# Kernel optimization log

Hardware: AMD Instinct MI355X
Metric: run time of the kernel (lower is better)

The kernel has to match this reference:

```python
import jax, jax.numpy as jnp
import numpy as np

N_HEADS = 16
NEG_INF = float('-inf')


def setup_inputs() -> dict:
    key = jax.random.key(0)
    ks = jax.random.split(key, 8)
    B, S, D = 8, 1024, 1024
    inp = {
        'q': jax.random.normal(ks[0], (B, S, D), jnp.float32),
        'k': jax.random.normal(ks[1], (B, S, D), jnp.float32),
        'v': jax.random.normal(ks[2], (B, S, D), jnp.float32),
        'key_padding_mask': jnp.zeros((B, S), bool),
        'Wq': jax.random.normal(ks[3], (D, D), jnp.float32) / np.sqrt(D),
        'bq': jnp.zeros((D,), jnp.float32),
        'Wk': jax.random.normal(ks[4], (D, D), jnp.float32) / np.sqrt(D),
        'bk': jnp.zeros((D,), jnp.float32),
        'Wv': jax.random.normal(ks[5], (D, D), jnp.float32) / np.sqrt(D),
        'bv': jnp.zeros((D,), jnp.float32),
        'Wo': jax.random.normal(ks[6], (D, D), jnp.float32) / np.sqrt(D),
        'bo': jnp.zeros((D,), jnp.float32),
    }
    return inp


def reference(q, k, v, key_padding_mask, Wq, bq, Wk, bk, Wv, bv, Wo, bo):
    B, T, D = q.shape
    S = k.shape[1]
    H = N_HEADS
    dh = D // H
    causal = True

    # projections (torch Linear: x @ W.T + b)
    qh = (q @ Wq.T + bq).reshape(B, T, H, dh).transpose(0, 2, 1, 3)  # b h t d
    kh = (k @ Wk.T + bk).reshape(B, S, H, dh).transpose(0, 2, 1, 3)  # b h s d
    vh = (v @ Wv.T + bv).reshape(B, S, H, dh).transpose(0, 2, 1, 3)  # b h s d

    s = jnp.einsum('bhtd,bhsd->bhts', qh, kh) / jnp.sqrt(jnp.asarray(dh, s_dtype(qh)))
    s = jnp.where(key_padding_mask[:, None, None, :], NEG_INF, s)
    if causal:
        cmask = jnp.triu(jnp.full((T, S), NEG_INF, s.dtype), 1)
        s = s + cmask[None, None]
    a = jax.nn.softmax(s.astype(jnp.float32), axis=-1).astype(s.dtype)
    o = jnp.einsum('bhts,bhsd->bhtd', a, vh)
    o = o.transpose(0, 2, 1, 3).reshape(B, T, D)
    return o @ Wo.T + bo


def s_dtype(x):
    return x.dtype
```

## Files before the change

kernel.cpp:

```cpp
#include <hip/hip_runtime.h>
#include <hip/hip_bf16.h>

typedef unsigned short u16;
typedef unsigned int u32;
typedef __attribute__((ext_vector_type(8))) short bf16x8;
typedef __attribute__((ext_vector_type(4))) float f32x4;

#define LOG2E 1.44269504088896340736f


__device__ inline u16 f2bf(float f) {
  union { float f; u32 u; } v; v.f = f;
  u32 r = v.u + 0x7fffu + ((v.u >> 16) & 1u);
  return (u16)(r >> 16);
}

__device__ inline void gload_lds16(const u16* g, u16* l) {
  __builtin_amdgcn_global_load_lds(
      (const __attribute__((address_space(1))) u32*)g,
      (__attribute__((address_space(3))) u32*)l, 16, 0, 0);
}


__global__ void cvt_multi(const float4* __restrict__ s0, const float4* __restrict__ s1,
                          const float4* __restrict__ s2, const float4* __restrict__ s3,
                          ushort4* __restrict__ d0, ushort4* __restrict__ d1,
                          ushort4* __restrict__ d2, ushort4* __restrict__ d3, int n4) {
  const float4* s; ushort4* d;
  switch (blockIdx.y) {
    case 0: s = s0; d = d0; break;
    case 1: s = s1; d = d1; break;
    case 2: s = s2; d = d2; break;
    default: s = s3; d = d3; break;
  }
  int stride = gridDim.x * blockDim.x;
  for (int i = blockIdx.x * blockDim.x + threadIdx.x; i < n4; i += stride) {
    float4 v = s[i];
    ushort4 o;
    o.x = f2bf(v.x); o.y = f2bf(v.y); o.z = f2bf(v.z); o.w = f2bf(v.w);
    d[i] = o;
  }
}


__global__ void mask_flags(const unsigned char* __restrict__ mask,
                           unsigned char* __restrict__ flags) {
  int t = threadIdx.x;
  if (t >= 128) return;
  const uint4* p = (const uint4*)(mask + (size_t)t * 64);
  uint4 a = p[0], b = p[1], c = p[2], d = p[3];
  u32 v = a.x | a.y | a.z | a.w | b.x | b.y | b.z | b.w |
          c.x | c.y | c.z | c.w | d.x | d.y | d.z | d.w;
  flags[t] = v ? 1 : 0;
}


template<int MODE>
__global__ __launch_bounds__(256) void gemm_nt_bf16(
    const u16* __restrict__ A, const u16* __restrict__ Bt,
    const float* __restrict__ bias, void* __restrict__ Cout,
    int M, int N, int K) {
  constexpr int BK = 32;
  __shared__ u16 sA[2][128 * BK];
  __shared__ u16 sB[2][128 * BK];

  const int tid = threadIdx.x;
  const int lane = tid & 63;
  const int wave = tid >> 6;
  const int g = lane >> 4;
  const int r = lane & 15;
  const int wr = wave >> 1, wc = wave & 1;
  const int m0 = blockIdx.y * 128, n0 = blockIdx.x * 128;

  f32x4 acc[4][4] = {};

  auto stage = [&](int buf, int kt) {
    const int k0 = kt * BK;
#pragma unroll
    for (int i = 0; i < 2; ++i) {
      int c = tid + i * 256;
      int row = c >> 2, cc = c & 3;
      gload_lds16(A + (size_t)(m0 + row) * K + k0 + cc * 8, &sA[buf][0] + c * 8);
    }
#pragma unroll
    for (int i = 0; i < 2; ++i) {
      int c = tid + i * 256;
      int row = c >> 2, cc = c & 3;
      gload_lds16(Bt + (size_t)(n0 + row) * K + k0 + cc * 8, &sB[buf][0] + c * 8);
    }
  };

  stage(0, 0);
  const int NT = K / BK;
  for (int kt = 0; kt < NT; ++kt) {
    __syncthreads();
    if (kt + 1 < NT) stage((kt + 1) & 1, kt + 1);
    const u16* a_base = &sA[kt & 1][0];
    const u16* b_base = &sB[kt & 1][0];
    bf16x8 avf[4], bvf[4];
#pragma unroll
    for (int i = 0; i < 4; ++i) {
      avf[i] = *(const bf16x8*)(a_base + (wr * 64 + i * 16 + r) * BK + g * 8);
      bvf[i] = *(const bf16x8*)(b_base + (wc * 64 + i * 16 + r) * BK + g * 8);
    }
#pragma unroll
    for (int i = 0; i < 4; ++i)
#pragma unroll
      for (int j = 0; j < 4; ++j)
        acc[i][j] = __builtin_amdgcn_mfma_f32_16x16x32_bf16(avf[i], bvf[j], acc[i][j], 0, 0, 0);
  }

#pragma unroll
  for (int i = 0; i < 4; ++i) {
    int rowb = m0 + wr * 64 + i * 16 + g * 4;
#pragma unroll
    for (int j = 0; j < 4; ++j) {
      int col = n0 + wc * 64 + j * 16 + r;
      float bv = bias[col];
#pragma unroll
      for (int q = 0; q < 4; ++q) {
        int row = rowb + q;
        float v = acc[i][j][q] + bv;
        if (MODE == 0) {
          ((float*)Cout)[(size_t)row * N + col] = v;
        } else if (MODE == 1) {
          int b = row >> 10, t = row & 1023, h = col >> 6, d = col & 63;
          ((u16*)Cout)[((((size_t)b * 16 + h) << 10) + t) * 64 + d] = f2bf(v);
        } else {
          int b = row >> 10, s = row & 1023, h = col >> 6, d = col & 63;
          ((u16*)Cout)[(((size_t)b * 16 + h) * 64 + d) * 1024 + s] = f2bf(v);
        }
      }
    }
  }
}


__global__ __launch_bounds__(256) void gemm_qkv(
    const u16* __restrict__ Aq, const u16* __restrict__ Ak, const u16* __restrict__ Av,
    const u16* __restrict__ Wqb, const u16* __restrict__ Wkb, const u16* __restrict__ Wvb,
    const float* __restrict__ bqp, const float* __restrict__ bkp, const float* __restrict__ bvp,
    u16* __restrict__ Qh, u16* __restrict__ Kh, u16* __restrict__ Vt,
    int M, int N, int K) {
  constexpr int BK = 32;
  __shared__ u16 sA[2][128 * BK];
  __shared__ u16 sB[2][128 * BK];

  const int z = blockIdx.z;
  const u16* A  = (z == 0) ? Aq : (z == 1) ? Ak : Av;
  const u16* Bt = (z == 0) ? Wqb : (z == 1) ? Wkb : Wvb;
  const float* bias = (z == 0) ? bqp : (z == 1) ? bkp : bvp;

  const int tid = threadIdx.x;
  const int lane = tid & 63;
  const int wave = tid >> 6;
  const int g = lane >> 4;
  const int r = lane & 15;
  const int wr = wave >> 1, wc = wave & 1;
  const int m0 = blockIdx.y * 128, n0 = blockIdx.x * 128;

  f32x4 acc[4][4] = {};

  auto stage = [&](int buf, int kt) {
    const int k0 = kt * BK;
#pragma unroll
    for (int i = 0; i < 2; ++i) {
      int c = tid + i * 256;
      int row = c >> 2, cc = c & 3;
      gload_lds16(A + (size_t)(m0 + row) * K + k0 + cc * 8, &sA[buf][0] + c * 8);
    }
#pragma unroll
    for (int i = 0; i < 2; ++i) {
      int c = tid + i * 256;
      int row = c >> 2, cc = c & 3;
      gload_lds16(Bt + (size_t)(n0 + row) * K + k0 + cc * 8, &sB[buf][0] + c * 8);
    }
  };

  stage(0, 0);
  const int NT = K / BK;
  for (int kt = 0; kt < NT; ++kt) {
    __syncthreads();
    if (kt + 1 < NT) stage((kt + 1) & 1, kt + 1);
    const u16* a_base = &sA[kt & 1][0];
    const u16* b_base = &sB[kt & 1][0];
    bf16x8 avf[4], bvf[4];
#pragma unroll
    for (int i = 0; i < 4; ++i) {
      avf[i] = *(const bf16x8*)(a_base + (wr * 64 + i * 16 + r) * BK + g * 8);
      bvf[i] = *(const bf16x8*)(b_base + (wc * 64 + i * 16 + r) * BK + g * 8);
    }
#pragma unroll
    for (int i = 0; i < 4; ++i)
#pragma unroll
      for (int j = 0; j < 4; ++j)
        acc[i][j] = __builtin_amdgcn_mfma_f32_16x16x32_bf16(avf[i], bvf[j], acc[i][j], 0, 0, 0);
  }

#pragma unroll
  for (int i = 0; i < 4; ++i) {
    int rowb = m0 + wr * 64 + i * 16 + g * 4;
#pragma unroll
    for (int j = 0; j < 4; ++j) {
      int col = n0 + wc * 64 + j * 16 + r;
      float bv = bias[col];
#pragma unroll
      for (int q = 0; q < 4; ++q) {
        int row = rowb + q;
        float v = acc[i][j][q] + bv;
        int b = row >> 10, t = row & 1023, h = col >> 6, d = col & 63;
        if (z <= 1) {
          u16* dst = (z == 0) ? Qh : Kh;
          dst[((((size_t)b * 16 + h) << 10) + t) * 64 + d] = f2bf(v);
        } else {
          Vt[(((size_t)b * 16 + h) * 64 + d) * 1024 + t] = f2bf(v);
        }
      }
    }
  }
}


__global__ __launch_bounds__(256) void attn_fwd(
    const u16* __restrict__ Qh, const u16* __restrict__ Kh,
    const u16* __restrict__ Vt, const unsigned char* __restrict__ mask,
    const unsigned char* __restrict__ padflags,
    u16* __restrict__ O) {
  constexpr int S = 1024, DH = 64;
  __shared__ u16 sK[2][64 * 64];
  __shared__ u16 sV[2][64 * 64];
  __shared__ u16 sP[4][16 * 64];

  const int tid = threadIdx.x, lane = tid & 63, wave = tid >> 6;
  const int g = lane >> 4, r = lane & 15;
  const int bh = blockIdx.x;
  const int qt = blockIdx.y;
  const int b = bh >> 4, h = bh & 15;
  const int qw = qt * 128 + wave * 32;

  bf16x8 qf[2][2];
#pragma unroll
  for (int u = 0; u < 2; ++u) {
    const u16* Qb = Qh + ((size_t)bh * S + qw + u * 16 + r) * DH;
    qf[u][0] = *(const bf16x8*)(Qb + g * 8);
    qf[u][1] = *(const bf16x8*)(Qb + 32 + g * 8);
  }

  f32x4 acc[2][4] = {};
  float mrun[2][4], lrun[2][4];
#pragma unroll
  for (int u = 0; u < 2; ++u)
#pragma unroll
    for (int i = 0; i < 4; ++i) { mrun[u][i] = -INFINITY; lrun[u][i] = 0.f; }

  auto stage = [&](int buf, int kvt) {
    const int s0k = kvt * 64;
#pragma unroll
    for (int i = 0; i < 2; ++i) {
      int c = tid + i * 256;
      int row = c >> 3;
      int cc = (c & 7) ^ (row & 7);
      gload_lds16(Kh + ((size_t)bh * S + s0k + row) * DH + cc * 8, &sK[buf][0] + c * 8);
      gload_lds16(Vt + ((size_t)bh * DH + row) * S + s0k + cc * 8, &sV[buf][0] + c * 8);
    }
  };

  const int NT = 2 * (qt + 1);
  stage(0, 0);
  for (int kvt = 0; kvt < NT; ++kvt) {
    __syncthreads();
    if (kvt + 1 < NT) stage((kvt + 1) & 1, kvt + 1);
    const int cur = kvt & 1;
    const int s0 = kvt * 64;
    const bool pad = padflags[b * 16 + (s0 >> 6)] != 0;
    const u16* Kb = &sK[cur][0];
    const u16* Vb = &sV[cur][0];
    u16* Pw = &sP[wave][0];

#pragma unroll
    for (int u = 0; u < 2; ++u) {
      const int qg = qw + u * 16;
      if (s0 > qg + 15) continue;
      const bool diag = (s0 + 63 > qg);

      f32x4 sc[4] = {};
#pragma unroll
      for (int ss = 0; ss < 4; ++ss) {
#pragma unroll
        for (int kc = 0; kc < 2; ++kc) {
          int krow = ss * 16 + r;
          int byteoff = krow * 128 + kc * 64 + g * 16;
          bf16x8 kf = *(const bf16x8*)((const char*)Kb + (byteoff ^ ((krow & 7) << 4)));
          sc[ss] = __builtin_amdgcn_mfma_f32_16x16x32_bf16(qf[u][kc], kf, sc[ss], 0, 0, 0);
        }
      }

      float sv[4][4];
      float pmax[4] = {-INFINITY, -INFINITY, -INFINITY, -INFINITY};
#pragma unroll
      for (int ss = 0; ss < 4; ++ss) {
        float padd = 0.f;
        if (pad) {
          int s_g = s0 + ss * 16 + r;
          if (mask[(size_t)b * S + s_g]) padd = -INFINITY;
        }
#pragma unroll
        for (int reg = 0; reg < 4; ++reg) {
          float v = sc[ss][reg] * (0.125f * LOG2E) + padd;
          if (diag) {
            int s_g = s0 + ss * 16 + r;
            int q_g = qg + g * 4 + reg;
            if (s_g > q_g) v = -INFINITY;
          }
          sv[ss][reg] = v;
          pmax[reg] = fmaxf(pmax[reg], v);
        }
      }
#pragma unroll
      for (int reg = 0; reg < 4; ++reg) {
        float m = pmax[reg];
        m = fmaxf(m, __shfl_xor(m, 1));
        m = fmaxf(m, __shfl_xor(m, 2));
        m = fmaxf(m, __shfl_xor(m, 4));
        m = fmaxf(m, __shfl_xor(m, 8));
        float newm = fmaxf(mrun[u][reg], m);
        float alpha = (newm == -INFINITY) ? 1.f : exp2f(mrun[u][reg] - newm);
        mrun[u][reg] = newm;
        float rs = 0.f;
#pragma unroll
        for (int ss = 0; ss < 4; ++ss) {
          float p = (newm == -INFINITY) ? 0.f : exp2f(sv[ss][reg] - newm);
          sv[ss][reg] = p;
          rs += p;
        }
        rs += __shfl_xor(rs, 1);
        rs += __shfl_xor(rs, 2);
        rs += __shfl_xor(rs, 4);
        rs += __shfl_xor(rs, 8);
        lrun[u][reg] = lrun[u][reg] * alpha + rs;
#pragma unroll
        for (int df = 0; df < 4; ++df) acc[u][df][reg] *= alpha;
      }

#pragma unroll
      for (int ss = 0; ss < 4; ++ss) {
#pragma unroll
        for (int reg = 0; reg < 4; ++reg) {
          int qrow = g * 4 + reg;
          int byteoff = qrow * 128 + (ss * 16 + r) * 2;
          *(u16*)((char*)Pw + (byteoff ^ ((qrow & 7) << 4))) = f2bf(sv[ss][reg]);
        }
      }

#pragma unroll
      for (int sc2 = 0; sc2 < 2; ++sc2) {
        int pbyte = r * 128 + sc2 * 64 + g * 16;
        bf16x8 pf = *(const bf16x8*)((const char*)Pw + (pbyte ^ ((r & 7) << 4)));
#pragma unroll
        for (int df = 0; df < 4; ++df) {
          int vrow = df * 16 + r;
          int vbyte = vrow * 128 + sc2 * 64 + g * 16;
          bf16x8 vf = *(const bf16x8*)((const char*)Vb + (vbyte ^ ((vrow & 7) << 4)));
          acc[u][df] = __builtin_amdgcn_mfma_f32_16x16x32_bf16(pf, vf, acc[u][df], 0, 0, 0);
        }
      }
    }
  }

#pragma unroll
  for (int u = 0; u < 2; ++u) {
#pragma unroll
    for (int reg = 0; reg < 4; ++reg) {
      float l = lrun[u][reg];
      float inv = (l > 0.f) ? 1.f / l : 0.f;
      int t = qw + u * 16 + g * 4 + reg;
#pragma unroll
      for (int df = 0; df < 4; ++df) {
        float vo = acc[u][df][reg] * inv;
        O[((size_t)b * 1024 + t) * 1024 + h * 64 + df * 16 + r] = f2bf(vo);
      }
    }
  }
}


extern "C" void kernel_launch(void* const* d_in, const int* in_sizes, int n_in,
                              void* d_out, int out_size, void* d_ws, size_t ws_size,
                              hipStream_t stream) {
  const float* q  = (const float*)d_in[0];
  const float* k  = (const float*)d_in[1];
  const float* v  = (const float*)d_in[2];
  const unsigned char* mask = (const unsigned char*)d_in[3];
  const float* Wq = (const float*)d_in[4];
  const float* bq = (const float*)d_in[5];
  const float* Wk = (const float*)d_in[6];
  const float* bk = (const float*)d_in[7];
  const float* Wv = (const float*)d_in[8];
  const float* bv = (const float*)d_in[9];
  const float* Wo = (const float*)d_in[10];
  const float* bo = (const float*)d_in[11];

  const int M = 8192, N = 1024, K = 1024;
  const size_t MB = 1u << 20;
  char* ws = (char*)d_ws;

  if (ws_size >= 104 * MB + 4096) {
    u16* Aq  = (u16*)(ws);
    u16* Ak  = (u16*)(ws + 16 * MB);
    u16* Av  = (u16*)(ws + 32 * MB);
    u16* Qh  = (u16*)(ws + 48 * MB);
    u16* Kh  = (u16*)(ws + 64 * MB);
    u16* Vt  = (u16*)(ws + 80 * MB);
    u16* Wqb = (u16*)(ws + 96 * MB);
    u16* Wkb = Wqb + (1u << 20);
    u16* Wvb = Wkb + (1u << 20);
    u16* Wob = Wvb + (1u << 20);
    unsigned char* flags = (unsigned char*)(ws + 104 * MB);
    u16* AttO = Aq;

    cvt_multi<<<dim3(1024, 3), 256, 0, stream>>>(
        (const float4*)q, (const float4*)k, (const float4*)v, (const float4*)q,
        (ushort4*)Aq, (ushort4*)Ak, (ushort4*)Av, (ushort4*)Aq, (M * K) / 4);
    cvt_multi<<<dim3(256, 4), 256, 0, stream>>>(
        (const float4*)Wq, (const float4*)Wk, (const float4*)Wv, (const float4*)Wo,
        (ushort4*)Wqb, (ushort4*)Wkb, (ushort4*)Wvb, (ushort4*)Wob, (N * K) / 4);
    mask_flags<<<1, 128, 0, stream>>>(mask, flags);

    gemm_qkv<<<dim3(N / 128, M / 128, 3), 256, 0, stream>>>(
        Aq, Ak, Av, Wqb, Wkb, Wvb, bq, bk, bv, Qh, Kh, Vt, M, N, K);

    attn_fwd<<<dim3(128, 8), 256, 0, stream>>>(Qh, Kh, Vt, mask, flags, AttO);

    gemm_nt_bf16<0><<<dim3(N / 128, M / 128), 256, 0, stream>>>(
        AttO, Wob, bo, (float*)d_out, M, N, K);
  } else {
    u16* wsA = (u16*)ws;
    u16* Qh  = (u16*)(ws + 16 * MB);
    u16* Kh  = (u16*)(ws + 32 * MB);
    u16* Vt  = (u16*)(ws + 48 * MB);
    u16* Wqb = (u16*)(ws + 64 * MB);
    u16* Wkb = Wqb + (1u << 20);
    u16* Wvb = Wkb + (1u << 20);
    u16* Wob = Wvb + (1u << 20);
    unsigned char* flags = (unsigned char*)(ws + 72 * MB);

    cvt_multi<<<dim3(256, 4), 256, 0, stream>>>(
        (const float4*)Wq, (const float4*)Wk, (const float4*)Wv, (const float4*)Wo,
        (ushort4*)Wqb, (ushort4*)Wkb, (ushort4*)Wvb, (ushort4*)Wob, (N * K) / 4);
    mask_flags<<<1, 128, 0, stream>>>(mask, flags);

    cvt_multi<<<dim3(1024, 1), 256, 0, stream>>>(
        (const float4*)q, (const float4*)q, (const float4*)q, (const float4*)q,
        (ushort4*)wsA, (ushort4*)wsA, (ushort4*)wsA, (ushort4*)wsA, (M * K) / 4);
    gemm_nt_bf16<1><<<dim3(N / 128, M / 128), 256, 0, stream>>>(wsA, Wqb, bq, Qh, M, N, K);
    cvt_multi<<<dim3(1024, 1), 256, 0, stream>>>(
        (const float4*)k, (const float4*)k, (const float4*)k, (const float4*)k,
        (ushort4*)wsA, (ushort4*)wsA, (ushort4*)wsA, (ushort4*)wsA, (M * K) / 4);
    gemm_nt_bf16<1><<<dim3(N / 128, M / 128), 256, 0, stream>>>(wsA, Wkb, bk, Kh, M, N, K);
    cvt_multi<<<dim3(1024, 1), 256, 0, stream>>>(
        (const float4*)v, (const float4*)v, (const float4*)v, (const float4*)v,
        (ushort4*)wsA, (ushort4*)wsA, (ushort4*)wsA, (ushort4*)wsA, (M * K) / 4);
    gemm_nt_bf16<2><<<dim3(N / 128, M / 128), 256, 0, stream>>>(wsA, Wvb, bv, Vt, M, N, K);

    attn_fwd<<<dim3(128, 8), 256, 0, stream>>>(Qh, Kh, Vt, mask, flags, wsA);

    gemm_nt_bf16<0><<<dim3(N / 128, M / 128), 256, 0, stream>>>(
        wsA, Wob, bo, (float*)d_out, M, N, K);
  }
}
```

Before: 261.1 us.

## Fold softmax scale into Q projection, use DPP reductions, reverse causal tile order

The softmax scale (1/sqrt(dh)·log2e) is now applied once in the Q projection epilogue instead of on every score element in the attention loop. The cross-lane row max/sum reductions switch from ds_swizzle-based shuffles to DPP row_shr moves. Causal query tiles are launched in reverse so the heavy tiles start first and load balances better. P is converted to bf16 by truncation instead of round-to-nearest, which adds a small precision bias. Scaling Q before rounding it to bf16 also changes rounding slightly.

```diff
diff --git a/kernel.cpp b/kernel.cpp
--- a/kernel.cpp
+++ b/kernel.cpp
@@ -7,6 +7,7 @@
 typedef __attribute__((ext_vector_type(4))) float f32x4;
 
 #define LOG2E 1.44269504088896340736f
+#define QSCALE (0.125f * LOG2E)
 
 
 __device__ inline u16 f2bf(float f) {
@@ -19,6 +20,27 @@
   __builtin_amdgcn_global_load_lds(
       (const __attribute__((address_space(1))) u32*)g,
       (__attribute__((address_space(3))) u32*)l, 16, 0, 0);
+}
+
+template<int CTRL>
+__device__ inline float dppmov(float x) {
+  int i = __builtin_bit_cast(int, x);
+  int r = __builtin_amdgcn_update_dpp(i, i, CTRL, 0xf, 0xf, false);
+  return __builtin_bit_cast(float, r);
+}
+__device__ inline float rowmax16(float v) {
+  v = fmaxf(v, dppmov<0x128>(v));
+  v = fmaxf(v, dppmov<0x124>(v));
+  v = fmaxf(v, dppmov<0x122>(v));
+  v = fmaxf(v, dppmov<0x121>(v));
+  return v;
+}
+__device__ inline float rowsum16(float v) {
+  v += dppmov<0x128>(v);
+  v += dppmov<0x124>(v);
+  v += dppmov<0x122>(v);
+  v += dppmov<0x121>(v);
+  return v;
 }
 
 
@@ -123,7 +145,8 @@
         float v = acc[i][j][q] + bv;
         if (MODE == 0) {
           ((float*)Cout)[(size_t)row * N + col] = v;
-        } else if (MODE == 1) {
+        } else if (MODE == 1 || MODE == 3) {
+          if (MODE == 3) v *= QSCALE;
           int b = row >> 10, t = row & 1023, h = col >> 6, d = col & 63;
           ((u16*)Cout)[((((size_t)b * 16 + h) << 10) + t) * 64 + d] = f2bf(v);
         } else {
@@ -209,9 +232,10 @@
         int row = rowb + q;
         float v = acc[i][j][q] + bv;
         int b = row >> 10, t = row & 1023, h = col >> 6, d = col & 63;
-        if (z <= 1) {
-          u16* dst = (z == 0) ? Qh : Kh;
-          dst[((((size_t)b * 16 + h) << 10) + t) * 64 + d] = f2bf(v);
+        if (z == 0) {
+          Qh[((((size_t)b * 16 + h) << 10) + t) * 64 + d] = f2bf(v * QSCALE);
+        } else if (z == 1) {
+          Kh[((((size_t)b * 16 + h) << 10) + t) * 64 + d] = f2bf(v);
         } else {
           Vt[(((size_t)b * 16 + h) * 64 + d) * 1024 + t] = f2bf(v);
         }
@@ -234,7 +258,7 @@
   const int tid = threadIdx.x, lane = tid & 63, wave = tid >> 6;
   const int g = lane >> 4, r = lane & 15;
   const int bh = blockIdx.x;
-  const int qt = blockIdx.y;
+  const int qt = (int)gridDim.y - 1 - (int)blockIdx.y;
   const int b = bh >> 4, h = bh & 15;
   const int qw = qt * 128 + wave * 32;
 
@@ -306,7 +330,7 @@
         }
 #pragma unroll
         for (int reg = 0; reg < 4; ++reg) {
-          float v = sc[ss][reg] * (0.125f * LOG2E) + padd;
+          float v = sc[ss][reg] + padd;
           if (diag) {
             int s_g = s0 + ss * 16 + r;
             int q_g = qg + g * 4 + reg;
@@ -318,11 +342,7 @@
       }
 #pragma unroll
       for (int reg = 0; reg < 4; ++reg) {
-        float m = pmax[reg];
-        m = fmaxf(m, __shfl_xor(m, 1));
-        m = fmaxf(m, __shfl_xor(m, 2));
-        m = fmaxf(m, __shfl_xor(m, 4));
-        m = fmaxf(m, __shfl_xor(m, 8));
+        float m = rowmax16(pmax[reg]);
         float newm = fmaxf(mrun[u][reg], m);
         float alpha = (newm == -INFINITY) ? 1.f : exp2f(mrun[u][reg] - newm);
         mrun[u][reg] = newm;
@@ -333,10 +353,7 @@
           sv[ss][reg] = p;
           rs += p;
         }
-        rs += __shfl_xor(rs, 1);
-        rs += __shfl_xor(rs, 2);
-        rs += __shfl_xor(rs, 4);
-        rs += __shfl_xor(rs, 8);
+        rs = rowsum16(rs);
         lrun[u][reg] = lrun[u][reg] * alpha + rs;
 #pragma unroll
         for (int df = 0; df < 4; ++df) acc[u][df][reg] *= alpha;
@@ -348,7 +365,8 @@
         for (int reg = 0; reg < 4; ++reg) {
           int qrow = g * 4 + reg;
           int byteoff = qrow * 128 + (ss * 16 + r) * 2;
-          *(u16*)((char*)Pw + (byteoff ^ ((qrow & 7) << 4))) = f2bf(sv[ss][reg]);
+          u32 bits = __builtin_bit_cast(u32, sv[ss][reg]);
+          *(u16*)((char*)Pw + (byteoff ^ ((qrow & 7) << 4))) = (u16)(bits >> 16);
         }
       }
 
@@ -452,7 +470,7 @@
     cvt_multi<<<dim3(1024, 1), 256, 0, stream>>>(
         (const float4*)q, (const float4*)q, (const float4*)q, (const float4*)q,
         (ushort4*)wsA, (ushort4*)wsA, (ushort4*)wsA, (ushort4*)wsA, (M * K) / 4);
-    gemm_nt_bf16<1><<<dim3(N / 128, M / 128), 256, 0, stream>>>(wsA, Wqb, bq, Qh, M, N, K);
+    gemm_nt_bf16<3><<<dim3(N / 128, M / 128), 256, 0, stream>>>(wsA, Wqb, bq, Qh, M, N, K);
     cvt_multi<<<dim3(1024, 1), 256, 0, stream>>>(
         (const float4*)k, (const float4*)k, (const float4*)k, (const float4*)k,
         (ushort4*)wsA, (ushort4*)wsA, (ushort4*)wsA, (ushort4*)wsA, (M * K) / 4);
```

Measured after the change: 227.5 us. -12.9%, faster.
